# Optimization experiments

Measured on AMD Instinct MI355X. Metric: run time of the kernel, lower is better.

## Reference

```python
import jax, jax.numpy as jnp
import numpy as np

N, E, F, H, A = 100000, 1600000, 256, 32, 64


def setup_inputs() -> dict:
    key = jax.random.key(0)
    ks = jax.random.split(key, 14)
    s = lambda k, shp, scale: (jax.random.normal(k, shp, dtype=jnp.float32) * scale)
    return {
        "features": jax.random.normal(ks[0], (N, F), dtype=jnp.float32),
        "edge_index": jax.random.randint(ks[1], (2, E), 0, N, dtype=jnp.int64),
        "W1": s(ks[2], (F, H), 1.0 / np.sqrt(F)), "b1": jnp.zeros((H,), jnp.float32),
        "W2": s(ks[3], (H, H), 1.0 / np.sqrt(H)), "b2": jnp.zeros((H,), jnp.float32),
        "pW1": s(ks[4], (H, 512), 1.0 / np.sqrt(H)), "pb1": jnp.zeros((512,), jnp.float32),
        "pW2": s(ks[5], (512, A), 1.0 / np.sqrt(512)), "pb2": jnp.zeros((A,), jnp.float32),
        "vW1": s(ks[6], (H, 512), 1.0 / np.sqrt(H)), "vb1": jnp.zeros((512,), jnp.float32),
        "vW2": s(ks[7], (512, 1), 1.0 / np.sqrt(512)), "vb2": jnp.zeros((1,), jnp.float32),
    }


def _gcn_conv(x, src, dst, W, b, n):
    # PyG GCNConv: x' = D^{-1/2} (A+I) D^{-1/2} (x W) + b  (self-loops already in src/dst)
    x = x @ W  # [n, out]
    deg = jax.ops.segment_sum(jnp.ones(src.shape[0], x.dtype), dst, num_segments=n)
    dinv = jnp.where(deg > 0, jax.lax.rsqrt(jnp.maximum(deg, 1e-12)), 0.0).astype(x.dtype)
    norm = dinv[src] * dinv[dst]                       # [E+n]
    msg = x[src] * norm[:, None]                       # gather + scale
    return jax.ops.segment_sum(msg, dst, num_segments=n) + b  # scatter-add


def reference(features, edge_index, W1, b1, W2, b2, pW1, pb1, pW2, pb2, vW1, vb1, vW2, vb2):
    n = features.shape[0]
    loop = jnp.arange(n, dtype=edge_index.dtype)
    src = jnp.concatenate([edge_index[0], loop])
    dst = jnp.concatenate([edge_index[1], loop])
    h = jax.nn.relu(_gcn_conv(features, src, dst, W1, b1, n))
    h = jax.nn.relu(_gcn_conv(h, src, dst, W2, b2, n))  # [n, H] == conv_out
    policy = jax.nn.relu(h @ pW1 + pb1) @ pW2 + pb2     # [n, A]
    value = jax.nn.relu(h @ vW1 + vb1) @ vW2 + vb2      # [n, 1]
    return policy, value
```

## Files before the change

### kernel.cpp

```cpp
#include <hip/hip_runtime.h>

#define FDIM 256
#define HDIM 32
#define D1   512
#define ADIM 64
#define BKT_SHIFT 9
#define BKT_NODES 512

typedef __bf16 bf16x8 __attribute__((ext_vector_type(8)));
typedef float  f32x4  __attribute__((ext_vector_type(4)));

__device__ __forceinline__ float bf2f(unsigned short h){
  unsigned int u = ((unsigned int)h) << 16;
  return __builtin_bit_cast(float, u);
}
__device__ __forceinline__ unsigned short f2bf(float f){
  unsigned int u = __builtin_bit_cast(unsigned int, f);
  u = u + 0x7fff + ((u >> 16) & 1u);
  return (unsigned short)(u >> 16);
}

__global__ void k_zero(int* bktot){
  bktot[threadIdx.x] = 0;
}

__global__ __launch_bounds__(256) void k_hist(const int* __restrict__ dst,
                                              int* __restrict__ bktot, int e){
  __shared__ int h[256];
  int t = threadIdx.x; h[t] = 0; __syncthreads();
  for (int i = blockIdx.x*256 + t; i < e; i += gridDim.x*256)
    atomicAdd(&h[dst[i] >> BKT_SHIFT], 1);
  __syncthreads();
  if (h[t]) atomicAdd(&bktot[t], h[t]);
}

__global__ void k_bscan(const int* __restrict__ bktot, int* __restrict__ bkbase,
                        int* __restrict__ bkcur, int* __restrict__ rowptr,
                        int nbk, int n, int e){
  __shared__ int s[256];
  int t = threadIdx.x;
  int v = (t < nbk) ? bktot[t] : 0;
  s[t] = v; __syncthreads();
  for (int off = 1; off < 256; off <<= 1){
    int tv = (t >= off) ? s[t-off] : 0; __syncthreads();
    s[t] += tv; __syncthreads();
  }
  bkbase[t] = s[t] - v;
  bkcur[t]  = s[t] - v;
  if (t == 0){ bkbase[nbk] = e; rowptr[n] = e; }
}

__global__ __launch_bounds__(256) void k_stage(const int* __restrict__ src,
                                               const int* __restrict__ dst,
                                               int* __restrict__ bkcur,
                                               uint2* __restrict__ stage, int e){
  __shared__ int h[256], base[256], cur[256];
  int t = threadIdx.x;
  h[t] = 0; cur[t] = 0;
  __syncthreads();
  int lo = blockIdx.x*8192, hi = min(e, lo + 8192);
  for (int i = lo + t; i < hi; i += 256)
    atomicAdd(&h[dst[i] >> BKT_SHIFT], 1);
  __syncthreads();
  if (h[t] > 0) base[t] = atomicAdd(&bkcur[t], h[t]);
  __syncthreads();
  for (int i = lo + t; i < hi; i += 256){
    int d = dst[i]; int b = d >> BKT_SHIFT;
    int r = atomicAdd(&cur[b], 1);
    stage[base[b] + r] = make_uint2((unsigned)src[i], (unsigned)d);
  }
}

__global__ __launch_bounds__(256) void k_fine(const uint2* __restrict__ stage,
                                              const int* __restrict__ bkbase,
                                              int* __restrict__ rowptr,
                                              int* __restrict__ col,
                                              float* __restrict__ dinv, int n){
  __shared__ int h[512], ofs[512], s[256];
  int b = blockIdx.x, t = threadIdx.x;
  int e0 = bkbase[b], e1 = bkbase[b+1];
  int nb0 = b << BKT_SHIFT;
  h[t] = 0; h[t+256] = 0; __syncthreads();
  for (int i = e0 + t; i < e1; i += 256)
    atomicAdd(&h[(int)stage[i].y - nb0], 1);
  __syncthreads();
  int a0 = h[2*t], a1 = h[2*t+1], v = a0 + a1;
  s[t] = v; __syncthreads();
  for (int off = 1; off < 256; off <<= 1){
    int tv = (t >= off) ? s[t-off] : 0; __syncthreads();
    s[t] += tv; __syncthreads();
  }
  int ex = s[t] - v;
  ofs[2*t] = ex; ofs[2*t+1] = ex + a0;
  int node0 = nb0 + 2*t, node1 = node0 + 1;
  if (node0 < n){ rowptr[node0] = e0 + ex;      dinv[node0] = rsqrtf((float)(a0 + 1)); }
  if (node1 < n){ rowptr[node1] = e0 + ex + a0; dinv[node1] = rsqrtf((float)(a1 + 1)); }
  __syncthreads();
  for (int i = e0 + t; i < e1; i += 256){
    uint2 u = stage[i];
    int r = atomicAdd(&ofs[(int)u.y - nb0], 1);
    col[e0 + r] = (int)u.x;
  }
}

__device__ __forceinline__ void prep_one(int i, const float* __restrict__ src,
                                         unsigned short* __restrict__ dst,
                                         int nnt, int ld, int ncols){
  int j = i & 7; int L = (i >> 3) & 63; int t = i >> 9;
  int nt = t % nnt; int kb = t / nnt;
  int k = kb*32 + ((L >> 4) * 8) + j;
  int n = nt*16 + (L & 15);
  float v = (n < ncols) ? src[k*ld + n] : 0.f;
  dst[i] = f2bf(v);
}

__global__ void k_prep(const float* W1, const float* W2, const float* pW1,
                       const float* vW1, const float* pW2, const float* vW2,
                       unsigned short* W1P, unsigned short* W2P, unsigned short* pW1P,
                       unsigned short* vW1P, unsigned short* pW2P, unsigned short* vW2P){
  int i = blockIdx.x*256 + threadIdx.x;
  if (i < 8192) { prep_one(i, W1,  W1P,  2, 32, 32);   return; } i -= 8192;
  if (i < 1024) { prep_one(i, W2,  W2P,  2, 32, 32);   return; } i -= 1024;
  if (i < 16384){ prep_one(i, pW1, pW1P, 32, 512, 512); return; } i -= 16384;
  if (i < 16384){ prep_one(i, vW1, vW1P, 32, 512, 512); return; } i -= 16384;
  if (i < 32768){ prep_one(i, pW2, pW2P, 4, 64, 64);   return; } i -= 32768;
  if (i < 8192) { prep_one(i, vW2, vW2P, 1, 1, 1);     return; }
}

__global__ __launch_bounds__(256) void k_gemm1(const float* __restrict__ feat,
                                               const unsigned short* __restrict__ W1P,
                                               const float* __restrict__ dinv,
                                               unsigned short* __restrict__ x1, int n){
  int lane = threadIdx.x & 63; int wv = threadIdx.x >> 6;
  int lid = lane & 15, quad = lane >> 4;
  int base = (blockIdx.x*4 + wv) * 16;
  int row = base + lid; if (row >= n) row = n - 1;
  const float* fr = feat + (size_t)row * FDIM;
  f32x4 acc0 = {0.f,0.f,0.f,0.f}, acc1 = {0.f,0.f,0.f,0.f};
#pragma unroll
  for (int kb = 0; kb < 8; ++kb){
    float4 fa = *(const float4*)(fr + kb*32 + quad*8);
    float4 fb = *(const float4*)(fr + kb*32 + quad*8 + 4);
    bf16x8 bfr;
    bfr[0]=(__bf16)fa.x; bfr[1]=(__bf16)fa.y; bfr[2]=(__bf16)fa.z; bfr[3]=(__bf16)fa.w;
    bfr[4]=(__bf16)fb.x; bfr[5]=(__bf16)fb.y; bfr[6]=(__bf16)fb.z; bfr[7]=(__bf16)fb.w;
    bf16x8 w0 = *(const bf16x8*)(W1P + (size_t)((kb*2+0)*64 + lane)*8);
    bf16x8 w1 = *(const bf16x8*)(W1P + (size_t)((kb*2+1)*64 + lane)*8);
    acc0 = __builtin_amdgcn_mfma_f32_16x16x32_bf16(w0, bfr, acc0, 0,0,0);
    acc1 = __builtin_amdgcn_mfma_f32_16x16x32_bf16(w1, bfr, acc1, 0,0,0);
  }
  if (base + lid < n){
    float di = dinv[base + lid];
    unsigned short* o = x1 + (size_t)(base+lid)*HDIM;
    uint2 p0, p1;
    p0.x = f2bf(acc0[0]*di) | ((unsigned)f2bf(acc0[1]*di)<<16);
    p0.y = f2bf(acc0[2]*di) | ((unsigned)f2bf(acc0[3]*di)<<16);
    p1.x = f2bf(acc1[0]*di) | ((unsigned)f2bf(acc1[1]*di)<<16);
    p1.y = f2bf(acc1[2]*di) | ((unsigned)f2bf(acc1[3]*di)<<16);
    *(uint2*)(o + quad*4)      = p0;
    *(uint2*)(o + 16 + quad*4) = p1;
  }
}

__global__ __launch_bounds__(256) void k_conv(const unsigned short* __restrict__ x,
                                              const float* __restrict__ dinv,
                                              const int* __restrict__ rowptr,
                                              const int* __restrict__ col,
                                              const float* __restrict__ bias,
                                              unsigned short* __restrict__ y, int n){
  int node = (blockIdx.x*256 + threadIdx.x) >> 6;
  if (node >= n) return;
  int lane = threadIdx.x & 63;
  int c = lane & 31, eh = lane >> 5;
  float acc = (eh == 0) ? bf2f(x[(size_t)node*HDIM + c]) : 0.f;
  int s0 = rowptr[node], s1 = rowptr[node+1];
  int nfull = (s1 - s0) >> 3;
  int jb = s0 + (eh << 2);
#pragma clang loop unroll_count(2)
  for (int t = 0; t < nfull; ++t, jb += 8){
    int c0 = col[jb+0], c1 = col[jb+1], c2 = col[jb+2], c3 = col[jb+3];
    float v0 = bf2f(x[(size_t)c0*HDIM + c]);
    float v1 = bf2f(x[(size_t)c1*HDIM + c]);
    float v2 = bf2f(x[(size_t)c2*HDIM + c]);
    float v3 = bf2f(x[(size_t)c3*HDIM + c]);
    acc += (v0 + v1) + (v2 + v3);
  }
  for (int j = s0 + nfull*8 + eh; j < s1; j += 2){
    int s = col[j];
    acc += bf2f(x[(size_t)s*HDIM + c]);
  }
  acc += __shfl_xor(acc, 32);
  if (eh == 0){
    float v = acc * dinv[node] + bias[c];
    y[(size_t)node*HDIM + c] = f2bf(fmaxf(v, 0.f));
  }
}

__global__ __launch_bounds__(256) void k_gemm2(const unsigned short* __restrict__ h1,
                                               const unsigned short* __restrict__ W2P,
                                               const float* __restrict__ dinv,
                                               unsigned short* __restrict__ x2, int n){
  int lane = threadIdx.x & 63; int wv = threadIdx.x >> 6;
  int lid = lane & 15, quad = lane >> 4;
  int base = (blockIdx.x*4 + wv) * 16;
  int row = base + lid; if (row >= n) row = n - 1;
  bf16x8 hb = *(const bf16x8*)(h1 + (size_t)row*HDIM + quad*8);
  bf16x8 w0 = *(const bf16x8*)(W2P + (size_t)(0*64 + lane)*8);
  bf16x8 w1 = *(const bf16x8*)(W2P + (size_t)(1*64 + lane)*8);
  f32x4 z = {0.f,0.f,0.f,0.f};
  f32x4 a0 = __builtin_amdgcn_mfma_f32_16x16x32_bf16(w0, hb, z, 0,0,0);
  f32x4 a1 = __builtin_amdgcn_mfma_f32_16x16x32_bf16(w1, hb, z, 0,0,0);
  if (base + lid < n){
    float di = dinv[base + lid];
    unsigned short* o = x2 + (size_t)(base+lid)*HDIM;
    uint2 p0, p1;
    p0.x = f2bf(a0[0]*di) | ((unsigned)f2bf(a0[1]*di)<<16);
    p0.y = f2bf(a0[2]*di) | ((unsigned)f2bf(a0[3]*di)<<16);
    p1.x = f2bf(a1[0]*di) | ((unsigned)f2bf(a1[1]*di)<<16);
    p1.y = f2bf(a1[2]*di) | ((unsigned)f2bf(a1[3]*di)<<16);
    *(uint2*)(o + quad*4)      = p0;
    *(uint2*)(o + 16 + quad*4) = p1;
  }
}

__global__ __launch_bounds__(256) void k_head(const unsigned short* __restrict__ h,
    const unsigned short* __restrict__ pW1P, const unsigned short* __restrict__ pW2P,
    const unsigned short* __restrict__ vW1P, const unsigned short* __restrict__ vW2P,
    const float* __restrict__ pb1, const float* __restrict__ pb2,
    const float* __restrict__ vb1, const float* __restrict__ vb2,
    float* __restrict__ pol, float* __restrict__ val, int n){
  __shared__ unsigned short lds[4*16*520];
  int lane = threadIdx.x & 63; int wv = threadIdx.x >> 6;
  int lid = lane & 15, quad = lane >> 4;
  int nbase = (blockIdx.x*4 + wv) * 16;
  unsigned short* tl = lds + wv*16*520;
  int hrow = nbase + lid; if (hrow >= n) hrow = n - 1;
  bf16x8 hfrag = *(const bf16x8*)(h + (size_t)hrow*HDIM + quad*8);
  f32x4 z = {0.f,0.f,0.f,0.f};

#pragma unroll 4
  for (int t = 0; t < 32; ++t){
    bf16x8 a = *(const bf16x8*)(pW1P + (size_t)(t*64 + lane)*8);
    f32x4 c = __builtin_amdgcn_mfma_f32_16x16x32_bf16(a, hfrag, z, 0,0,0);
    float4 b = *(const float4*)(pb1 + t*16 + quad*4);
    uint2 p;
    p.x = f2bf(fmaxf(c[0]+b.x,0.f)) | ((unsigned)f2bf(fmaxf(c[1]+b.y,0.f))<<16);
    p.y = f2bf(fmaxf(c[2]+b.z,0.f)) | ((unsigned)f2bf(fmaxf(c[3]+b.w,0.f))<<16);
    *(uint2*)(tl + lid*520 + t*16 + quad*4) = p;
  }
  {
    f32x4 acc[4] = {z,z,z,z};
#pragma unroll 4
    for (int kb = 0; kb < 16; ++kb){
      bf16x8 a = *(const bf16x8*)(tl + lid*520 + kb*32 + quad*8);
#pragma unroll
      for (int tt = 0; tt < 4; ++tt){
        bf16x8 b = *(const bf16x8*)(pW2P + (size_t)((kb*4+tt)*64 + lane)*8);
        acc[tt] = __builtin_amdgcn_mfma_f32_16x16x32_bf16(a, b, acc[tt], 0,0,0);
      }
    }
#pragma unroll
    for (int tt = 0; tt < 4; ++tt){
      float pb2v = pb2[tt*16 + lid];
#pragma unroll
      for (int r = 0; r < 4; ++r){
        int node = nbase + quad*4 + r;
        if (node < n) pol[(size_t)node*ADIM + tt*16 + lid] = acc[tt][r] + pb2v;
      }
    }
  }
#pragma unroll 4
  for (int t = 0; t < 32; ++t){
    bf16x8 a = *(const bf16x8*)(vW1P + (size_t)(t*64 + lane)*8);
    f32x4 c = __builtin_amdgcn_mfma_f32_16x16x32_bf16(a, hfrag, z, 0,0,0);
    float4 b = *(const float4*)(vb1 + t*16 + quad*4);
    uint2 p;
    p.x = f2bf(fmaxf(c[0]+b.x,0.f)) | ((unsigned)f2bf(fmaxf(c[1]+b.y,0.f))<<16);
    p.y = f2bf(fmaxf(c[2]+b.z,0.f)) | ((unsigned)f2bf(fmaxf(c[3]+b.w,0.f))<<16);
    *(uint2*)(tl + lid*520 + t*16 + quad*4) = p;
  }
  {
    f32x4 acc = z;
#pragma unroll 4
    for (int kb = 0; kb < 16; ++kb){
      bf16x8 a = *(const bf16x8*)(tl + lid*520 + kb*32 + quad*8);
      bf16x8 b = *(const bf16x8*)(vW2P + (size_t)(kb*64 + lane)*8);
      acc = __builtin_amdgcn_mfma_f32_16x16x32_bf16(a, b, acc, 0,0,0);
    }
    if (lid == 0){
      float vb = vb2[0];
#pragma unroll
      for (int r = 0; r < 4; ++r){
        int node = nbase + quad*4 + r;
        if (node < n) val[node] = acc[r] + vb;
      }
    }
  }
}

extern "C" void kernel_launch(void* const* d_in, const int* in_sizes, int n_in,
                              void* d_out, int out_size, void* d_ws, size_t ws_size,
                              hipStream_t stream){
  const float* feat = (const float*)d_in[0];
  const int*   edge = (const int*)d_in[1];
  const float* W1  = (const float*)d_in[2];
  const float* b1  = (const float*)d_in[3];
  const float* W2  = (const float*)d_in[4];
  const float* b2  = (const float*)d_in[5];
  const float* pW1 = (const float*)d_in[6];
  const float* pb1 = (const float*)d_in[7];
  const float* pW2 = (const float*)d_in[8];
  const float* pb2 = (const float*)d_in[9];
  const float* vW1 = (const float*)d_in[10];
  const float* vb1 = (const float*)d_in[11];
  const float* vW2 = (const float*)d_in[12];
  const float* vb2 = (const float*)d_in[13];
  int n = in_sizes[0] / FDIM;
  int e = in_sizes[1] / 2;
  int nbk = (n + BKT_NODES - 1) >> BKT_SHIFT;

  char* w = (char*)d_ws;
  auto alloc = [&](size_t bytes)->char*{
    char* p = w; w += (bytes + 255) & ~(size_t)255; return p;
  };
  size_t nodebuf = (size_t)n*HDIM*2;
  size_t stagesz = (size_t)e*8;
  char* stagebuf = alloc(stagesz > 2*nodebuf ? stagesz : 2*nodebuf);
  uint2* stage = (uint2*)stagebuf;
  unsigned short* x1 = (unsigned short*)stagebuf;
  unsigned short* h1 = (unsigned short*)(stagebuf + nodebuf);
  int*   col    = (int*)  alloc((size_t)e*4);
  int*   rowptr = (int*)  alloc((size_t)(n+1)*4);
  float* dinv   = (float*)alloc((size_t)n*4);
  int*   bktot  = (int*)  alloc(256*4);
  int*   bkbase = (int*)  alloc(257*4);
  int*   bkcur  = (int*)  alloc(256*4);
  unsigned short* W1P  = (unsigned short*)alloc(8192*2);
  unsigned short* W2P  = (unsigned short*)alloc(1024*2);
  unsigned short* pW1P = (unsigned short*)alloc(16384*2);
  unsigned short* vW1P = (unsigned short*)alloc(16384*2);
  unsigned short* pW2P = (unsigned short*)alloc(32768*2);
  unsigned short* vW2P = (unsigned short*)alloc(8192*2);

  int gb = (n + 63)/64;

  k_zero <<<1, 256, 0, stream>>>(bktot);
  k_hist <<<256, 256, 0, stream>>>(edge + e, bktot, e);
  k_bscan<<<1, 256, 0, stream>>>(bktot, bkbase, bkcur, rowptr, nbk, n, e);
  k_stage<<<(e + 8191)/8192, 256, 0, stream>>>(edge, edge + e, bkcur, stage, e);
  k_fine <<<nbk, 256, 0, stream>>>(stage, bkbase, rowptr, col, dinv, n);
  k_prep <<<(82944 + 255)/256, 256, 0, stream>>>(W1, W2, pW1, vW1, pW2, vW2,
                                                 W1P, W2P, pW1P, vW1P, pW2P, vW2P);
  k_gemm1<<<gb, 256, 0, stream>>>(feat, W1P, dinv, x1, n);
  k_conv <<<(n + 3)/4, 256, 0, stream>>>(x1, dinv, rowptr, col, b1, h1, n);
  k_gemm2<<<gb, 256, 0, stream>>>(h1, W2P, dinv, x1, n);
  k_conv <<<(n + 3)/4, 256, 0, stream>>>(x1, dinv, rowptr, col, b2, h1, n);
  float* pol = (float*)d_out;
  float* val = pol + (size_t)n*ADIM;
  k_head <<<gb, 256, 0, stream>>>(h1, pW1P, pW2P, vW1P, vW2P,
                                  pb1, pb2, vb1, vb2, pol, val, n);
}
```

Before: 444.7 us.

## Interleave policy head layers via small LDS ring and compute value head with FMA

The policy head now computes each 32-wide slice of the 512-wide hidden layer and consumes it right away in the second-layer MFMAs, using a double-buffered per-wave LDS tile of 16x56 instead of a 16x520 staging buffer. This cuts LDS per block from about 66 KB to about 14 KB so more blocks fit per CU (launch bounds now request 4). The value head drops its padded MFMA second layer (1 useful column out of 16) for a per-lane FP32 dot product with the raw vW2, reduced with two cross-lane shuffles, and its bf16 prep is removed. A cheaper round-half-up bf16 pack replaces round-to-nearest-even, which can change rounding slightly.

New measurement: 429.9 us. 3.3% less time.

```diff
diff --git a/kernel.cpp b/kernel.cpp
--- a/kernel.cpp
+++ b/kernel.cpp
@@ -18,6 +18,11 @@
   unsigned int u = __builtin_bit_cast(unsigned int, f);
   u = u + 0x7fff + ((u >> 16) & 1u);
   return (unsigned short)(u >> 16);
+}
+__device__ __forceinline__ unsigned int pk2(float a, float b){
+  unsigned int ua = __builtin_bit_cast(unsigned int, a) + 0x8000u;
+  unsigned int ub = __builtin_bit_cast(unsigned int, b) + 0x8000u;
+  return (ua >> 16) | (ub & 0xffff0000u);
 }
 
 __global__ void k_zero(int* bktot){
@@ -115,16 +120,15 @@
 }
 
 __global__ void k_prep(const float* W1, const float* W2, const float* pW1,
-                       const float* vW1, const float* pW2, const float* vW2,
+                       const float* vW1, const float* pW2,
                        unsigned short* W1P, unsigned short* W2P, unsigned short* pW1P,
-                       unsigned short* vW1P, unsigned short* pW2P, unsigned short* vW2P){
+                       unsigned short* vW1P, unsigned short* pW2P){
   int i = blockIdx.x*256 + threadIdx.x;
   if (i < 8192) { prep_one(i, W1,  W1P,  2, 32, 32);   return; } i -= 8192;
   if (i < 1024) { prep_one(i, W2,  W2P,  2, 32, 32);   return; } i -= 1024;
   if (i < 16384){ prep_one(i, pW1, pW1P, 32, 512, 512); return; } i -= 16384;
   if (i < 16384){ prep_one(i, vW1, vW1P, 32, 512, 512); return; } i -= 16384;
-  if (i < 32768){ prep_one(i, pW2, pW2P, 4, 64, 64);   return; } i -= 32768;
-  if (i < 8192) { prep_one(i, vW2, vW2P, 1, 1, 1);     return; }
+  if (i < 32768){ prep_one(i, pW2, pW2P, 4, 64, 64);   return; }
 }
 
 __global__ __launch_bounds__(256) void k_gemm1(const float* __restrict__ feat,
@@ -223,78 +227,71 @@
   }
 }
 
-__global__ __launch_bounds__(256) void k_head(const unsigned short* __restrict__ h,
+#define TSTR 56
+__global__ __launch_bounds__(256, 4) void k_head(const unsigned short* __restrict__ h,
     const unsigned short* __restrict__ pW1P, const unsigned short* __restrict__ pW2P,
-    const unsigned short* __restrict__ vW1P, const unsigned short* __restrict__ vW2P,
+    const unsigned short* __restrict__ vW1P, const float* __restrict__ vW2,
     const float* __restrict__ pb1, const float* __restrict__ pb2,
     const float* __restrict__ vb1, const float* __restrict__ vb2,
     float* __restrict__ pol, float* __restrict__ val, int n){
-  __shared__ unsigned short lds[4*16*520];
+  __shared__ unsigned short lds[4*2*16*TSTR];
   int lane = threadIdx.x & 63; int wv = threadIdx.x >> 6;
   int lid = lane & 15, quad = lane >> 4;
   int nbase = (blockIdx.x*4 + wv) * 16;
-  unsigned short* tl = lds + wv*16*520;
+  unsigned short* tb = lds + wv*(2*16*TSTR);
   int hrow = nbase + lid; if (hrow >= n) hrow = n - 1;
   bf16x8 hfrag = *(const bf16x8*)(h + (size_t)hrow*HDIM + quad*8);
   f32x4 z = {0.f,0.f,0.f,0.f};
-
-#pragma unroll 4
-  for (int t = 0; t < 32; ++t){
-    bf16x8 a = *(const bf16x8*)(pW1P + (size_t)(t*64 + lane)*8);
-    f32x4 c = __builtin_amdgcn_mfma_f32_16x16x32_bf16(a, hfrag, z, 0,0,0);
-    float4 b = *(const float4*)(pb1 + t*16 + quad*4);
-    uint2 p;
-    p.x = f2bf(fmaxf(c[0]+b.x,0.f)) | ((unsigned)f2bf(fmaxf(c[1]+b.y,0.f))<<16);
-    p.y = f2bf(fmaxf(c[2]+b.z,0.f)) | ((unsigned)f2bf(fmaxf(c[3]+b.w,0.f))<<16);
-    *(uint2*)(tl + lid*520 + t*16 + quad*4) = p;
-  }
-  {
-    f32x4 acc[4] = {z,z,z,z};
-#pragma unroll 4
-    for (int kb = 0; kb < 16; ++kb){
-      bf16x8 a = *(const bf16x8*)(tl + lid*520 + kb*32 + quad*8);
-#pragma unroll
-      for (int tt = 0; tt < 4; ++tt){
-        bf16x8 b = *(const bf16x8*)(pW2P + (size_t)((kb*4+tt)*64 + lane)*8);
-        acc[tt] = __builtin_amdgcn_mfma_f32_16x16x32_bf16(a, b, acc[tt], 0,0,0);
-      }
-    }
+  f32x4 acc[4] = {z,z,z,z};
+
+#pragma unroll 2
+  for (int kb = 0; kb < 16; ++kb){
+    unsigned short* buf = tb + (kb & 1)*16*TSTR;
+    bf16x8 w0 = *(const bf16x8*)(pW1P + (size_t)((2*kb+0)*64 + lane)*8);
+    bf16x8 w1 = *(const bf16x8*)(pW1P + (size_t)((2*kb+1)*64 + lane)*8);
+    f32x4 c0 = __builtin_amdgcn_mfma_f32_16x16x32_bf16(w0, hfrag, z, 0,0,0);
+    f32x4 c1 = __builtin_amdgcn_mfma_f32_16x16x32_bf16(w1, hfrag, z, 0,0,0);
+    float4 b0 = *(const float4*)(pb1 + (2*kb+0)*16 + quad*4);
+    float4 b1 = *(const float4*)(pb1 + (2*kb+1)*16 + quad*4);
+    uint2 p0, p1;
+    p0.x = pk2(fmaxf(c0[0]+b0.x,0.f), fmaxf(c0[1]+b0.y,0.f));
+    p0.y = pk2(fmaxf(c0[2]+b0.z,0.f), fmaxf(c0[3]+b0.w,0.f));
+    p1.x = pk2(fmaxf(c1[0]+b1.x,0.f), fmaxf(c1[1]+b1.y,0.f));
+    p1.y = pk2(fmaxf(c1[2]+b1.z,0.f), fmaxf(c1[3]+b1.w,0.f));
+    *(uint2*)(buf + lid*TSTR + quad*4)      = p0;
+    *(uint2*)(buf + lid*TSTR + 16 + quad*4) = p1;
+    bf16x8 a = *(const bf16x8*)(buf + lid*TSTR + quad*8);
 #pragma unroll
     for (int tt = 0; tt < 4; ++tt){
-      float pb2v = pb2[tt*16 + lid];
+      bf16x8 b = *(const bf16x8*)(pW2P + (size_t)((kb*4+tt)*64 + lane)*8);
+      acc[tt] = __builtin_amdgcn_mfma_f32_16x16x32_bf16(a, b, acc[tt], 0,0,0);
+    }
+  }
 #pragma unroll
-      for (int r = 0; r < 4; ++r){
-        int node = nbase + quad*4 + r;
-        if (node < n) pol[(size_t)node*ADIM + tt*16 + lid] = acc[tt][r] + pb2v;
-      }
+  for (int tt = 0; tt < 4; ++tt){
+    float pb2v = pb2[tt*16 + lid];
+#pragma unroll
+    for (int r = 0; r < 4; ++r){
+      int node = nbase + quad*4 + r;
+      if (node < n) pol[(size_t)node*ADIM + tt*16 + lid] = acc[tt][r] + pb2v;
     }
   }
+
+  float vacc = 0.f;
 #pragma unroll 4
   for (int t = 0; t < 32; ++t){
     bf16x8 a = *(const bf16x8*)(vW1P + (size_t)(t*64 + lane)*8);
     f32x4 c = __builtin_amdgcn_mfma_f32_16x16x32_bf16(a, hfrag, z, 0,0,0);
-    float4 b = *(const float4*)(vb1 + t*16 + quad*4);
-    uint2 p;
-    p.x = f2bf(fmaxf(c[0]+b.x,0.f)) | ((unsigned)f2bf(fmaxf(c[1]+b.y,0.f))<<16);
-    p.y = f2bf(fmaxf(c[2]+b.z,0.f)) | ((unsigned)f2bf(fmaxf(c[3]+b.w,0.f))<<16);
-    *(uint2*)(tl + lid*520 + t*16 + quad*4) = p;
-  }
-  {
-    f32x4 acc = z;
-#pragma unroll 4
-    for (int kb = 0; kb < 16; ++kb){
-      bf16x8 a = *(const bf16x8*)(tl + lid*520 + kb*32 + quad*8);
-      bf16x8 b = *(const bf16x8*)(vW2P + (size_t)(kb*64 + lane)*8);
-      acc = __builtin_amdgcn_mfma_f32_16x16x32_bf16(a, b, acc, 0,0,0);
-    }
-    if (lid == 0){
-      float vb = vb2[0];
-#pragma unroll
-      for (int r = 0; r < 4; ++r){
-        int node = nbase + quad*4 + r;
-        if (node < n) val[node] = acc[r] + vb;
-      }
-    }
+    float4 b  = *(const float4*)(vb1 + t*16 + quad*4);
+    float4 w2 = *(const float4*)(vW2 + t*16 + quad*4);
+    vacc += fmaxf(c[0]+b.x,0.f)*w2.x + fmaxf(c[1]+b.y,0.f)*w2.y
+          + fmaxf(c[2]+b.z,0.f)*w2.z + fmaxf(c[3]+b.w,0.f)*w2.w;
+  }
+  vacc += __shfl_xor(vacc, 16);
+  vacc += __shfl_xor(vacc, 32);
+  if (quad == 0){
+    int node = nbase + lid;
+    if (node < n) val[node] = vacc + vb2[0];
   }
 }
 
@@ -340,7 +337,6 @@
   unsigned short* pW1P = (unsigned short*)alloc(16384*2);
   unsigned short* vW1P = (unsigned short*)alloc(16384*2);
   unsigned short* pW2P = (unsigned short*)alloc(32768*2);
-  unsigned short* vW2P = (unsigned short*)alloc(8192*2);
 
   int gb = (n + 63)/64;
 
@@ -349,14 +345,14 @@
   k_bscan<<<1, 256, 0, stream>>>(bktot, bkbase, bkcur, rowptr, nbk, n, e);
   k_stage<<<(e + 8191)/8192, 256, 0, stream>>>(edge, edge + e, bkcur, stage, e);
   k_fine <<<nbk, 256, 0, stream>>>(stage, bkbase, rowptr, col, dinv, n);
-  k_prep <<<(82944 + 255)/256, 256, 0, stream>>>(W1, W2, pW1, vW1, pW2, vW2,
-                                                 W1P, W2P, pW1P, vW1P, pW2P, vW2P);
+  k_prep <<<(74752 + 255)/256, 256, 0, stream>>>(W1, W2, pW1, vW1, pW2,
+                                                 W1P, W2P, pW1P, vW1P, pW2P);
   k_gemm1<<<gb, 256, 0, stream>>>(feat, W1P, dinv, x1, n);
   k_conv <<<(n + 3)/4, 256, 0, stream>>>(x1, dinv, rowptr, col, b1, h1, n);
   k_gemm2<<<gb, 256, 0, stream>>>(h1, W2P, dinv, x1, n);
   k_conv <<<(n + 3)/4, 256, 0, stream>>>(x1, dinv, rowptr, col, b2, h1, n);
   float* pol = (float*)d_out;
   float* val = pol + (size_t)n*ADIM;
-  k_head <<<gb, 256, 0, stream>>>(h1, pW1P, pW2P, vW1P, vW2P,
+  k_head <<<gb, 256, 0, stream>>>(h1, pW1P, pW2P, vW1P, vW2,
                                   pb1, pb2, vb1, vb2, pol, val, n);
 }
```
